# Optimization experiments

Measured on AMD Instinct MI355X. Metric: run time of the kernel, lower is better.

The kernel has to match this reference:

```python
import jax, jax.numpy as jnp
import numpy as np

B, T_AUX, UP = 4, 75, 110
N_AUX, N_Q, HID, SKIP = 54, 256, 192, 256
K, AUX_K = 6, 3
DIL_FACTS = [0, 1, 2] * 3  # dilation_depth=3, dilation_repeat=3
T = T_AUX * UP - 1  # 8249


def conv1d(x, w, b, dil=1, pad=(0, 0)):
    # x: (B,C,T), w: (O,I,K) torch Conv1d layout
    if pad != (0, 0):
        x = jnp.pad(x, ((0, 0), (0, 0), pad))
    y = jax.lax.conv_general_dilated(x, w, (1,), 'VALID', rhs_dilation=(dil,),
                                     dimension_numbers=('NCH', 'OIH', 'NCH'))
    return y + b[None, :, None]


def setup_inputs() -> dict:
    key = jax.random.key(0)
    ks = jax.random.split(key, 24)
    s = 0.05
    inp = {
        'audio': jax.random.normal(ks[0], (B, N_Q, T), jnp.float32),
        'aux': jax.random.normal(ks[1], (B, N_AUX, T_AUX), jnp.float32),
        'scale_in_w': jax.random.normal(ks[2], (N_AUX, N_AUX, 1), jnp.float32) * s,
        'scale_in_b': jax.random.normal(ks[3], (N_AUX,), jnp.float32) * s,
        'aux0_w': jax.random.normal(ks[4], (N_AUX * 3, N_AUX, AUX_K), jnp.float32) * s,
        'aux0_b': jax.random.normal(ks[5], (N_AUX * 3,), jnp.float32) * s,
        'aux1_w': jax.random.normal(ks[6], (N_AUX * 9, N_AUX * 3, AUX_K), jnp.float32) * s,
        'aux1_b': jax.random.normal(ks[7], (N_AUX * 9,), jnp.float32) * s,
        'up_w': jax.random.normal(ks[8], (UP,), jnp.float32) * s,
        'up_b': jax.random.normal(ks[9], (), jnp.float32) * s,
        'causal_w': jax.random.normal(ks[10], (HID, N_Q, K), jnp.float32) * s,
        'causal_b': jax.random.normal(ks[11], (HID,), jnp.float32) * s,
        'inx_w': jax.random.normal(ks[12], (9, 2 * HID, N_AUX * 9, 1), jnp.float32) * s,
        'inx_b': jax.random.normal(ks[13], (9, 2 * HID), jnp.float32) * s,
        'dilh_w': jax.random.normal(ks[14], (9, 2 * HID, HID, K), jnp.float32) * s,
        'dilh_b': jax.random.normal(ks[15], (9, 2 * HID), jnp.float32) * s,
        'skip_w': jax.random.normal(ks[16], (9, SKIP, HID, 1), jnp.float32) * s,
        'skip_b': jax.random.normal(ks[17], (9, SKIP), jnp.float32) * s,
        'out1_w': jax.random.normal(ks[18], (N_Q, SKIP, 1), jnp.float32) * s,
        'out1_b': jax.random.normal(ks[19], (N_Q,), jnp.float32) * s,
        'out2_w': jax.random.normal(ks[20], (N_Q, N_Q, 1), jnp.float32) * s,
        'out2_b': jax.random.normal(ks[21], (N_Q,), jnp.float32) * s,
    }
    return inp


def reference(audio, aux, scale_in_w, scale_in_b, aux0_w, aux0_b, aux1_w, aux1_b,
              up_w, up_b, causal_w, causal_b, inx_w, inx_b, dilh_w, dilh_b,
              skip_w, skip_b, out1_w, out1_b, out2_w, out2_b):
    # conditioning path: scale_in -> two-sided dilated convs -> deconv upsample
    a = conv1d(aux, scale_in_w, scale_in_b)
    a = conv1d(a, aux0_w, aux0_b, dil=1, pad=(1, 1))      # k=3, dil=1, same length
    a = conv1d(a, aux1_w, aux1_b, dil=3, pad=(3, 3))      # k=3, dil=3, same length
    b_, c_, t_ = a.shape
    x = (a[:, :, :, None] * up_w).reshape(b_, c_, t_ * UP) + up_b  # ConvTranspose2d(1,1,(1,UP))
    x = x[:, :, 1:]  # (B, 486, T)
    # audio path: causal conv (left pad k-1) + softsign
    h = jax.nn.soft_sign(conv1d(audio, causal_w, causal_b, dil=1, pad=(K - 1, 0)))
    sum_out = None
    for l, d in enumerate(DIL_FACTS):
        dil = K ** d
        lpad = dil * (K - 1)  # k**(d+1) - k**d
        xh = conv1d(x, inx_w[l], inx_b[l]) * conv1d(h, dilh_w[l], dilh_b[l], dil=dil, pad=(lpad, 0))
        z = jax.nn.sigmoid(xh[:, :HID])
        h = (1.0 - z) * jnp.tanh(xh[:, HID:]) + z * h
        skip = conv1d(h, skip_w[l], skip_b[l])
        sum_out = skip if sum_out is None else sum_out + skip
    out = conv1d(jax.nn.relu(sum_out), out1_w, out1_b)
    out = conv1d(jax.nn.relu(out), out2_w, out2_b)
    return out.transpose(0, 2, 1)  # (B, T, n_quantize)
```

## Files before the change

### kernel.cpp

```cpp
#include <hip/hip_runtime.h>

#define TLEN 8249
#define TPAD 8320
#define NTILES 130
#define NTILES2 65
#define NB 4
#define NAUX 54
#define NQ 256
#define HID 192
#define NSKIP 256
#define KW 6
#define UPF 110
#define TAUX 75
#define PADR 180
#define HROWS (PADR + TPAD)

typedef __attribute__((ext_vector_type(8))) short bf16x8v;
typedef __attribute__((ext_vector_type(4))) float f32x4;

__device__ __forceinline__ unsigned short f2bf(float f) {
  unsigned int u = __float_as_uint(f);
  u += 0x7FFFu + ((u >> 16) & 1u);
  return (unsigned short)(u >> 16);
}

__device__ __forceinline__ f32x4 mfma16(bf16x8v a, bf16x8v b, f32x4 c) {
  return __builtin_amdgcn_mfma_f32_16x16x32_bf16(a, b, c, 0, 0, 0);
}

__global__ void prepack_kernel(
    const float* causal_w, const float* dilh_w, const float* skip_w,
    const float* out1_w, const float* out2_w,
    const float* inx_w, const float* inx_b, const float* up_b,
    unsigned short* pk_causal, unsigned short* pk_dilh, unsigned short* pk_skip,
    unsigned short* pk_out1, unsigned short* pk_out2, float* Cbuf)
{
  int i = blockIdx.x * blockDim.x + threadIdx.x;
  if (i < 9*6*6*24*64*8) {
    int t = i;
    int j = t & 7; t >>= 3;
    int lane = t & 63; t >>= 6;
    int nf = t % 24; t /= 24;
    int kc = t % 6; t /= 6;
    int tap = t % 6; t /= 6;
    int l = t;
    int oc = nf*16 + (lane & 15);
    int ic = kc*32 + ((lane >> 4) << 3) + j;
    pk_dilh[i] = f2bf(dilh_w[((l*384 + oc)*HID + ic)*KW + tap]);
  }
  if (i < 6*8*12*64*8) {
    int t = i;
    int j = t & 7; t >>= 3;
    int lane = t & 63; t >>= 6;
    int nf = t % 12; t /= 12;
    int kc = t % 8; t /= 8;
    int tap = t;
    int oc = nf*16 + (lane & 15);
    int ic = kc*32 + ((lane >> 4) << 3) + j;
    pk_causal[i] = f2bf(causal_w[(oc*NQ + ic)*KW + tap]);
  }
  if (i < 9*6*16*64*8) {
    int t = i;
    int j = t & 7; t >>= 3;
    int lane = t & 63; t >>= 6;
    int nf = t % 16; t /= 16;
    int kc = t % 6; t /= 6;
    int l = t;
    int sc = nf*16 + (lane & 15);
    int ic = kc*32 + ((lane >> 4) << 3) + j;
    pk_skip[i] = f2bf(skip_w[(l*NSKIP + sc)*HID + ic]);
  }
  if (i < 8*16*64*8) {
    int t = i;
    int j = t & 7; t >>= 3;
    int lane = t & 63; t >>= 6;
    int nf = t % 16; t /= 16;
    int kc = t;
    int oq = nf*16 + (lane & 15);
    int sc = kc*32 + ((lane >> 4) << 3) + j;
    pk_out1[i] = f2bf(out1_w[oq*NSKIP + sc]);
    pk_out2[i] = f2bf(out2_w[oq*NQ + sc]);
  }
  if (i < 9*384) {
    int l = i / 384, oc = i % 384;
    const float* wr = inx_w + (l*384 + oc)*486;
    float s = 0.f;
    for (int c = 0; c < 486; c++) s += wr[c];
    Cbuf[i] = up_b[0]*s + inx_b[i];
  }
}

__global__ void zpad_kernel(unsigned short* h_all) {
  int i = blockIdx.x*blockDim.x + threadIdx.x;
  if (i < 9*NB*PADR*HID) {
    int slab = i / (NB*PADR*HID), r = i % (NB*PADR*HID);
    int b = r / (PADR*HID), rr = r % (PADR*HID);
    h_all[((size_t)slab*NB + b)*HROWS*HID + rr] = 0;
  }
}

__global__ void aux1_kernel(const float* aux, const float* w, const float* bias, float* a1) {
  int q = blockIdx.x, b = blockIdx.y, co = threadIdx.x;
  if (co >= NAUX) return;
  float acc = bias[co];
  for (int ci = 0; ci < NAUX; ci++)
    acc += w[co*NAUX + ci] * aux[(b*NAUX + ci)*TAUX + q];
  a1[(b*NAUX + co)*TAUX + q] = acc;
}

__global__ void aux2_kernel(const float* a1, const float* w, const float* bias, float* a2) {
  __shared__ float s[3][NAUX];
  int q = blockIdx.x, b = blockIdx.y, tid = threadIdx.x;
  for (int i = tid; i < 3*NAUX; i += blockDim.x) {
    int k = i / NAUX, c = i % NAUX;
    int qq = q - 1 + k;
    s[k][c] = (qq >= 0 && qq < TAUX) ? a1[(b*NAUX + c)*TAUX + qq] : 0.f;
  }
  __syncthreads();
  int co = tid;
  if (co >= 162) return;
  float acc = bias[co];
  for (int c = 0; c < NAUX; c++)
    #pragma unroll
    for (int k = 0; k < 3; k++)
      acc += w[(co*NAUX + c)*3 + k] * s[k][c];
  a2[(b*162 + co)*TAUX + q] = acc;
}

__global__ void aux3_kernel(const float* a2, const float* w, const float* bias, float* a3) {
  __shared__ float s[3][162];
  int q = blockIdx.x, b = blockIdx.y, tid = threadIdx.x;
  for (int i = tid; i < 3*162; i += blockDim.x) {
    int k = i / 162, c = i % 162;
    int qq = q + 3*(k - 1);
    s[k][c] = (qq >= 0 && qq < TAUX) ? a2[(b*162 + c)*TAUX + qq] : 0.f;
  }
  __syncthreads();
  int co = tid;
  if (co >= 486) return;
  float acc = bias[co];
  for (int c = 0; c < 162; c++)
    #pragma unroll
    for (int k = 0; k < 3; k++)
      acc += w[(co*162 + c)*3 + k] * s[k][c];
  a3[(b*486 + co)*TAUX + q] = acc;
}

__global__ void g_kernel(const float* a3, const float* inx_w, float* G) {
  __shared__ float s[486][15];
  int q0 = blockIdx.x * 15, b = blockIdx.y, l = blockIdx.z;
  int tid = threadIdx.x;
  for (int i = tid; i < 486*15; i += 384) {
    int c = i / 15, qq = i % 15;
    s[c][qq] = a3[(b*486 + c)*TAUX + q0 + qq];
  }
  __syncthreads();
  int oc = tid;
  float acc[15];
  #pragma unroll
  for (int qq = 0; qq < 15; qq++) acc[qq] = 0.f;
  const float* wrow = inx_w + (l*384 + oc)*486;
  for (int c = 0; c < 486; c++) {
    float w = wrow[c];
    #pragma unroll
    for (int qq = 0; qq < 15; qq++) acc[qq] += w * s[c][qq];
  }
  for (int qq = 0; qq < 15; qq++)
    G[((size_t)(l*NB + b)*TAUX + q0 + qq)*384 + oc] = acc[qq];
}

__global__ __launch_bounds__(256, 2)
void causal_kernel(const float* audio, const unsigned short* pk, const float* cb,
                   unsigned short* hbf)
{
  __shared__ __align__(16) unsigned short sA[72*264];
  int b = blockIdx.y, t0 = blockIdx.x*64, tid = threadIdx.x;
  int wv = tid >> 6, lane = tid & 63, lanelo = lane & 15, lanehi = lane >> 4;

  for (int i = tid; i < 72*256; i += 256) {
    int ic = i / 72, tt = i % 72;
    int t = t0 - 5 + tt;
    float v = (t >= 0 && t < TLEN) ? audio[(size_t)(b*NQ + ic)*TLEN + t] : 0.f;
    sA[tt*264 + ic] = f2bf(v);
  }
  __syncthreads();

  f32x4 acc[4][3];
  f32x4 z4 = {0.f, 0.f, 0.f, 0.f};
  #pragma unroll
  for (int m = 0; m < 4; m++)
    #pragma unroll
    for (int i = 0; i < 3; i++) acc[m][i] = z4;

  for (int tap = 0; tap < 6; tap++) {
    for (int kc = 0; kc < 8; kc++) {
      bf16x8v A[4];
      int ko = kc*32 + (lanehi << 3);
      #pragma unroll
      for (int m = 0; m < 4; m++)
        A[m] = *(const bf16x8v*)&sA[(m*16 + lanelo + tap)*264 + ko];
      #pragma unroll
      for (int i = 0; i < 3; i++) {
        int nf = wv*3 + i;
        bf16x8v Bf = *(const bf16x8v*)&pk[(size_t)((((tap*8) + kc)*12 + nf)*64 + lane)*8];
        #pragma unroll
        for (int m = 0; m < 4; m++) acc[m][i] = mfma16(A[m], Bf, acc[m][i]);
      }
    }
  }

  unsigned short hv[4][3][4];
  #pragma unroll
  for (int m = 0; m < 4; m++)
    #pragma unroll
    for (int i = 0; i < 3; i++) {
      int oc = (wv*3 + i)*16 + lanelo;
      float bias = cb[oc];
      #pragma unroll
      for (int r = 0; r < 4; r++) {
        float v = acc[m][i][r] + bias;
        hv[m][i][r] = f2bf(v / (1.f + fabsf(v)));
      }
    }
  __syncthreads();
  #pragma unroll
  for (int m = 0; m < 4; m++)
    #pragma unroll
    for (int i = 0; i < 3; i++) {
      int oc = (wv*3 + i)*16 + lanelo;
      int cbh = oc >> 3, jh = oc & 7;
      #pragma unroll
      for (int r = 0; r < 4; r++) {
        int tl = m*16 + (lanehi << 2) + r;
        sA[tl*192 + ((cbh ^ (tl&7))<<3) + jh] = hv[m][i][r];
      }
    }
  __syncthreads();
  #pragma unroll
  for (int j = 0; j < 6; j++) {
    int c = tid + j*256, row = c/24, cbk = c%24;
    uint4 v = *(const uint4*)&sA[row*192 + ((cbk ^ (row&7))<<3)];
    *(uint4*)&hbf[(size_t)(b*HROWS + t0 + row + PADR)*HID + cbk*8] = v;
  }
}

__global__ __launch_bounds__(512, 2)
void layer_kernel(int dil,
                  const unsigned short* __restrict__ hin,
                  unsigned short* __restrict__ hout,
                  const unsigned short* __restrict__ pk_dilh_l,
                  const float* __restrict__ dilh_b_l,
                  const float* __restrict__ Gl, const float* __restrict__ Cl,
                  const float* __restrict__ up_w)
{
  extern __shared__ __align__(16) unsigned short flat[];
  int b = blockIdx.y, t0 = blockIdx.x*128, tid = threadIdx.x;
  int wv = tid >> 6, lane = tid & 63, lanelo = lane & 15, lanehi = lane >> 4;
  int mwv = wv >> 2, nwv = wv & 3;

  const size_t hbase = (size_t)b * HROWS * HID;
  int rowbase0 = t0 - 5*dil + PADR;
  int W = 128 + 5*dil;

  for (int c = tid; c < W*24; c += 512) {
    int row = c/24, cbk = c%24;
    uint4 v = *(const uint4*)&hin[hbase + (size_t)(rowbase0+row)*HID + cbk*8];
    *(uint4*)&flat[row*192 + ((cbk ^ (row&7))<<3)] = v;
  }
  __syncthreads();

  f32x4 accz[4][3], acct[4][3];
  f32x4 z4 = {0.f, 0.f, 0.f, 0.f};
  #pragma unroll
  for (int m = 0; m < 4; m++)
    #pragma unroll
    for (int i = 0; i < 3; i++) { accz[m][i] = z4; acct[m][i] = z4; }

  for (int tap = 0; tap < 6; tap++) {
    #pragma unroll
    for (int kc = 0; kc < 6; kc++) {
      bf16x8v A[4];
      #pragma unroll
      for (int m = 0; m < 4; m++) {
        int r = mwv*64 + m*16 + lanelo + tap*dil;
        int cbk = kc*4 + lanehi;
        A[m] = *(const bf16x8v*)&flat[r*192 + ((cbk ^ (r&7))<<3)];
      }
      #pragma unroll
      for (int i = 0; i < 3; i++) {
        const unsigned short* bp =
            &pk_dilh_l[(size_t)(((tap*6 + kc)*24 + nwv*3 + i)*64 + lane)*8];
        bf16x8v Bz = *(const bf16x8v*)bp;
        bf16x8v Bt = *(const bf16x8v*)(bp + 12*512);
        #pragma unroll
        for (int m = 0; m < 4; m++) {
          accz[m][i] = mfma16(A[m], Bz, accz[m][i]);
          acct[m][i] = mfma16(A[m], Bt, acct[m][i]);
        }
      }
    }
  }

  float izc[3], itc[3], bzc[3], btc[3];
  #pragma unroll
  for (int i = 0; i < 3; i++) {
    int ocz = (nwv*3 + i)*16 + lanelo;
    izc[i] = Cl[ocz];       itc[i] = Cl[192 + ocz];
    bzc[i] = dilh_b_l[ocz]; btc[i] = dilh_b_l[192 + ocz];
  }
  unsigned short hnv[4][4][3];
  #pragma unroll
  for (int m = 0; m < 4; m++) {
    #pragma unroll
    for (int r = 0; r < 4; r++) {
      int tl = mwv*64 + m*16 + (lanehi << 2) + r;
      int t = t0 + tl;
      int hr = tl + 5*dil;
      int tp1 = t + 1;
      int q = tp1 / UPF; if (q > TAUX - 1) q = TAUX - 1;
      int ui = tp1 - q*UPF; if (ui > UPF - 1) ui = UPF - 1;
      float u = up_w[ui];
      const float* Gb = Gl + (size_t)(b*TAUX + q)*384;
      #pragma unroll
      for (int i = 0; i < 3; i++) {
        int ocz = (nwv*3 + i)*16 + lanelo;
        float iz = u*Gb[ocz]       + izc[i];
        float it = u*Gb[192 + ocz] + itc[i];
        float xz = (accz[m][i][r] + bzc[i]) * iz;
        float xt = (acct[m][i][r] + btc[i]) * it;
        float z  = 1.f / (1.f + __expf(-xz));
        float e2 = __expf(2.f*xt);
        float th = 1.f - 2.f/(e2 + 1.f);
        int cbh = ocz >> 3, jh = ocz & 7;
        unsigned short hob = flat[hr*192 + ((cbh ^ (hr&7))<<3) + jh];
        float hold = __uint_as_float(((unsigned int)hob) << 16);
        hnv[m][r][i] = f2bf((1.f - z)*th + z*hold);
      }
    }
  }
  __syncthreads();
  #pragma unroll
  for (int m = 0; m < 4; m++) {
    #pragma unroll
    for (int r = 0; r < 4; r++) {
      int tl = mwv*64 + m*16 + (lanehi << 2) + r;
      #pragma unroll
      for (int i = 0; i < 3; i++) {
        int ocz = (nwv*3 + i)*16 + lanelo;
        int cbh = ocz >> 3, jh = ocz & 7;
        flat[tl*192 + ((cbh ^ (tl&7))<<3) + jh] = hnv[m][r][i];
      }
    }
  }
  __syncthreads();
  #pragma unroll
  for (int j = 0; j < 6; j++) {
    int c = tid + j*512, row = c/24, cbk = c%24;
    uint4 v = *(const uint4*)&flat[row*192 + ((cbk ^ (row&7))<<3)];
    *(uint4*)&hout[hbase + (size_t)(t0 + row + PADR)*HID + cbk*8] = v;
  }
}

__global__ __launch_bounds__(512, 2)
void tail_kernel(const unsigned short* __restrict__ h_all,
                 const unsigned short* __restrict__ pk_skip,
                 const float* __restrict__ skip_b,
                 const unsigned short* __restrict__ pk1, const float* __restrict__ b1,
                 const unsigned short* __restrict__ pk2, const float* __restrict__ b2,
                 float* __restrict__ dout)
{
  extern __shared__ __align__(16) unsigned short ss[];
  int b = blockIdx.y, t0 = blockIdx.x*128, tid = threadIdx.x;
  int wv = tid >> 6, lane = tid & 63, lanelo = lane & 15, lanehi = lane >> 4;
  int mwv = wv >> 2, nwv = wv & 3;
  const size_t HS = (size_t)NB * HROWS * HID;

  auto hsrc = [&](int l) {
    int slab = (l == 8) ? 0 : (l + 1);
    return h_all + (size_t)slab*HS + (size_t)b*HROWS*HID + (size_t)(t0 + PADR)*HID;
  };

  uint4 st[6];
  {
    const unsigned short* src = hsrc(0);
    #pragma unroll
    for (int j = 0; j < 6; j++) {
      int c = tid + j*512, row = c/24, cbk = c%24;
      st[j] = *(const uint4*)&src[(size_t)row*HID + cbk*8];
    }
    #pragma unroll
    for (int j = 0; j < 6; j++) {
      int c = tid + j*512, row = c/24, cbk = c%24;
      *(uint4*)&ss[row*192 + ((cbk ^ (row&7))<<3)] = st[j];
    }
  }

  f32x4 acc[4][4];
  f32x4 z4 = {0.f, 0.f, 0.f, 0.f};
  #pragma unroll
  for (int m = 0; m < 4; m++)
    #pragma unroll
    for (int i = 0; i < 4; i++) acc[m][i] = z4;

  for (int l = 0; l < 9; l++) {
    __syncthreads();
    if (l < 8) {
      const unsigned short* src = hsrc(l + 1);
      #pragma unroll
      for (int j = 0; j < 6; j++) {
        int c = tid + j*512, row = c/24, cbk = c%24;
        st[j] = *(const uint4*)&src[(size_t)row*HID + cbk*8];
      }
    }
    const unsigned short* bufc = ss + (l & 1)*(128*192);
    #pragma unroll
    for (int kc = 0; kc < 6; kc++) {
      bf16x8v A[4];
      #pragma unroll
      for (int m = 0; m < 4; m++) {
        int r = mwv*64 + m*16 + lanelo;
        int cbk = kc*4 + lanehi;
        A[m] = *(const bf16x8v*)&bufc[r*192 + ((cbk ^ (r&7))<<3)];
      }
      #pragma unroll
      for (int i = 0; i < 4; i++) {
        bf16x8v Bf = *(const bf16x8v*)
            &pk_skip[(size_t)(((l*6 + kc)*16 + nwv*4 + i)*64 + lane)*8];
        #pragma unroll
        for (int m = 0; m < 4; m++) acc[m][i] = mfma16(A[m], Bf, acc[m][i]);
      }
    }
    if (l < 8) {
      unsigned short* bufn = ss + ((l+1) & 1)*(128*192);
      #pragma unroll
      for (int j = 0; j < 6; j++) {
        int c = tid + j*512, row = c/24, cbk = c%24;
        *(uint4*)&bufn[row*192 + ((cbk ^ (row&7))<<3)] = st[j];
      }
    }
  }
  __syncthreads();

  #pragma unroll
  for (int i = 0; i < 4; i++) {
    int sc = (nwv*4 + i)*16 + lanelo;
    float bias = 0.f;
    #pragma unroll
    for (int l = 0; l < 9; l++) bias += skip_b[l*NSKIP + sc];
    #pragma unroll
    for (int m = 0; m < 4; m++) {
      #pragma unroll
      for (int r = 0; r < 4; r++) {
        int tl = mwv*64 + m*16 + (lanehi << 2) + r;
        float v = acc[m][i][r] + bias;
        ss[tl*264 + sc] = f2bf(fmaxf(v, 0.f));
      }
    }
  }
  __syncthreads();

  #pragma unroll
  for (int m = 0; m < 4; m++)
    #pragma unroll
    for (int i = 0; i < 4; i++) acc[m][i] = z4;
  for (int kc = 0; kc < 8; kc++) {
    bf16x8v A[4];
    int ko = kc*32 + (lanehi << 3);
    #pragma unroll
    for (int m = 0; m < 4; m++)
      A[m] = *(const bf16x8v*)&ss[(mwv*64 + m*16 + lanelo)*264 + ko];
    #pragma unroll
    for (int i = 0; i < 4; i++) {
      bf16x8v Bf = *(const bf16x8v*)&pk1[(size_t)((kc*16 + nwv*4 + i)*64 + lane)*8];
      #pragma unroll
      for (int m = 0; m < 4; m++) acc[m][i] = mfma16(A[m], Bf, acc[m][i]);
    }
  }
  __syncthreads();
  #pragma unroll
  for (int m = 0; m < 4; m++)
    #pragma unroll
    for (int i = 0; i < 4; i++) {
      int oq = (nwv*4 + i)*16 + lanelo;
      float bias = b1[oq];
      #pragma unroll
      for (int r = 0; r < 4; r++) {
        int tl = mwv*64 + m*16 + (lanehi << 2) + r;
        float v = acc[m][i][r] + bias;
        ss[tl*264 + oq] = f2bf(fmaxf(v, 0.f));
      }
    }
  __syncthreads();

  #pragma unroll
  for (int m = 0; m < 4; m++)
    #pragma unroll
    for (int i = 0; i < 4; i++) acc[m][i] = z4;
  for (int kc = 0; kc < 8; kc++) {
    bf16x8v A[4];
    int ko = kc*32 + (lanehi << 3);
    #pragma unroll
    for (int m = 0; m < 4; m++)
      A[m] = *(const bf16x8v*)&ss[(mwv*64 + m*16 + lanelo)*264 + ko];
    #pragma unroll
    for (int i = 0; i < 4; i++) {
      bf16x8v Bf = *(const bf16x8v*)&pk2[(size_t)((kc*16 + nwv*4 + i)*64 + lane)*8];
      #pragma unroll
      for (int m = 0; m < 4; m++) acc[m][i] = mfma16(A[m], Bf, acc[m][i]);
    }
  }
  float* so2 = (float*)ss;
  #pragma unroll
  for (int p = 0; p < 2; p++) {
    __syncthreads();
    if (mwv == p) {
      #pragma unroll
      for (int m = 0; m < 4; m++) {
        #pragma unroll
        for (int i = 0; i < 4; i++) {
          int oq = (nwv*4 + i)*16 + lanelo;
          float bias = b2[oq];
          #pragma unroll
          for (int r = 0; r < 4; r++) {
            int lr = m*16 + (lanehi << 2) + r;
            so2[lr*260 + oq] = acc[m][i][r] + bias;
          }
        }
      }
    }
    __syncthreads();
    #pragma unroll
    for (int j = 0; j < 8; j++) {
      int c = tid + j*512, row = c >> 6, ch = c & 63;
      int t = t0 + p*64 + row;
      if (t < TLEN) {
        uint4 v = *(const uint4*)&so2[row*260 + ch*4];
        *(uint4*)&dout[(size_t)(b*TLEN + t)*NQ + ch*4] = v;
      }
    }
  }
}

extern "C" void kernel_launch(void* const* d_in, const int* in_sizes, int n_in,
                              void* d_out, int out_size, void* d_ws, size_t ws_size,
                              hipStream_t stream)
{
  const float* audio      = (const float*)d_in[0];
  const float* aux        = (const float*)d_in[1];
  const float* scale_in_w = (const float*)d_in[2];
  const float* scale_in_b = (const float*)d_in[3];
  const float* aux0_w     = (const float*)d_in[4];
  const float* aux0_b     = (const float*)d_in[5];
  const float* aux1_w     = (const float*)d_in[6];
  const float* aux1_b     = (const float*)d_in[7];
  const float* up_w       = (const float*)d_in[8];
  const float* up_b       = (const float*)d_in[9];
  const float* causal_w   = (const float*)d_in[10];
  const float* causal_b   = (const float*)d_in[11];
  const float* inx_w      = (const float*)d_in[12];
  const float* inx_b      = (const float*)d_in[13];
  const float* dilh_w     = (const float*)d_in[14];
  const float* dilh_b     = (const float*)d_in[15];
  const float* skip_w     = (const float*)d_in[16];
  const float* skip_b     = (const float*)d_in[17];
  const float* out1_w     = (const float*)d_in[18];
  const float* out1_b     = (const float*)d_in[19];
  const float* out2_w     = (const float*)d_in[20];
  const float* out2_b     = (const float*)d_in[21];

  char* ws = (char*)d_ws;
  size_t off = 0;
  auto alloc = [&](size_t bytes) -> void* {
    void* p = ws + off;
    off += (bytes + 255) & ~(size_t)255;
    return p;
  };
  unsigned short* pk_causal = (unsigned short*)alloc((size_t)6*8*12*64*8*2);
  unsigned short* pk_dilh   = (unsigned short*)alloc((size_t)9*6*6*24*64*8*2);
  unsigned short* pk_skip   = (unsigned short*)alloc((size_t)9*6*16*64*8*2);
  unsigned short* pk_out1   = (unsigned short*)alloc((size_t)8*16*64*8*2);
  unsigned short* pk_out2   = (unsigned short*)alloc((size_t)8*16*64*8*2);
  float* Cbuf    = (float*)alloc((size_t)9*384*4);
  float* a1      = (float*)alloc((size_t)NB*NAUX*TAUX*4);
  float* a2      = (float*)alloc((size_t)NB*162*TAUX*4);
  float* a3      = (float*)alloc((size_t)NB*486*TAUX*4);
  float* Gbuf    = (float*)alloc((size_t)9*NB*TAUX*384*4);
  const size_t HS = (size_t)NB*HROWS*HID;
  unsigned short* h_all = (unsigned short*)alloc((size_t)9*HS*2);

  hipFuncSetAttribute((const void*)layer_kernel,
                      hipFuncAttributeMaxDynamicSharedMemorySize, 120000);
  hipFuncSetAttribute((const void*)tail_kernel,
                      hipFuncAttributeMaxDynamicSharedMemorySize, 98304);

  hipLaunchKernelGGL(prepack_kernel, dim3((9*6*6*24*64*8 + 255)/256), dim3(256), 0, stream,
                     causal_w, dilh_w, skip_w, out1_w, out2_w, inx_w, inx_b, up_b,
                     pk_causal, pk_dilh, pk_skip, pk_out1, pk_out2, Cbuf);
  hipLaunchKernelGGL(zpad_kernel, dim3((9*NB*PADR*HID + 255)/256), dim3(256), 0, stream,
                     h_all);
  hipLaunchKernelGGL(aux1_kernel, dim3(TAUX, NB), dim3(64), 0, stream,
                     aux, scale_in_w, scale_in_b, a1);
  hipLaunchKernelGGL(aux2_kernel, dim3(TAUX, NB), dim3(192), 0, stream,
                     a1, aux0_w, aux0_b, a2);
  hipLaunchKernelGGL(aux3_kernel, dim3(TAUX, NB), dim3(512), 0, stream,
                     a2, aux1_w, aux1_b, a3);
  hipLaunchKernelGGL(g_kernel, dim3(5, NB, 9), dim3(384), 0, stream,
                     a3, inx_w, Gbuf);
  hipLaunchKernelGGL(causal_kernel, dim3(NTILES, NB), dim3(256), 0, stream,
                     audio, pk_causal, causal_b, h_all );

  const int dils[9] = {1, 6, 36, 1, 6, 36, 1, 6, 36};
  for (int l = 0; l < 9; l++) {
    const unsigned short* hin = h_all + (size_t)l*HS;
    unsigned short* hout      = (l == 8) ? h_all : h_all + (size_t)(l+1)*HS;
    int ldsb = (128 + 5*dils[l]) * 192 * 2;
    hipLaunchKernelGGL(layer_kernel, dim3(NTILES2, NB), dim3(512), ldsb, stream,
                       dils[l], hin, hout,
                       pk_dilh + (size_t)l*6*6*24*64*8,
                       dilh_b + (size_t)l*384,
                       Gbuf + (size_t)l*NB*TAUX*384,
                       Cbuf + (size_t)l*384,
                       up_w);
  }

  hipLaunchKernelGGL(tail_kernel, dim3(NTILES2, NB), dim3(512), 98304, stream,
                     h_all, pk_skip, skip_b, pk_out1, out1_b, pk_out2, out2_b,
                     (float*)d_out);
}
```

Baseline: 991.7 us.

## Fuse all WaveNet layers and tail into one persistent kernel with grid barriers

Replaces the nine per-layer launches and the separate tail kernel with one persistent kernel of 208 blocks. Each block keeps its 160-step tile of h resident in LDS across layers and accumulates the skip projection in registers. Between layers it writes the tile to a ping-pong global slab and syncs via an atomic grid barrier; only the dilation halo is reloaded. This removes launch overhead and the nine-slab write-then-reread of h for the tail, but depends on all blocks being co-resident and serializes layers on barrier latency, with fewer blocks than the earlier 260-block launches.

Result: slower. 1.191 ms (+20.1%).

```diff
diff --git a/kernel.cpp b/kernel.cpp
--- a/kernel.cpp
+++ b/kernel.cpp
@@ -2,8 +2,9 @@
 
 #define TLEN 8249
 #define TPAD 8320
-#define NTILES 130
-#define NTILES2 65
+#define NTILES_C 130
+#define NTILES_P 52
+#define NBLK (NTILES_P*NB)
 #define NB 4
 #define NAUX 54
 #define NQ 256
@@ -26,6 +27,18 @@
 
 __device__ __forceinline__ f32x4 mfma16(bf16x8v a, bf16x8v b, f32x4 c) {
   return __builtin_amdgcn_mfma_f32_16x16x32_bf16(a, b, c, 0, 0, 0);
+}
+
+__device__ __forceinline__ void gridbar(unsigned int* cnt, unsigned int target, int tid) {
+  __syncthreads();
+  if (tid == 0) {
+    __threadfence();
+    __hip_atomic_fetch_add(cnt, 1u, __ATOMIC_ACQ_REL, __HIP_MEMORY_SCOPE_AGENT);
+    while (__hip_atomic_load(cnt, __ATOMIC_ACQUIRE, __HIP_MEMORY_SCOPE_AGENT) < target)
+      __builtin_amdgcn_s_sleep(2);
+    __threadfence();
+  }
+  __syncthreads();
 }
 
 __global__ void prepack_kernel(
@@ -90,12 +103,12 @@
   }
 }
 
-__global__ void zpad_kernel(unsigned short* h_all) {
+__global__ void zpad_kernel(unsigned short* s0, unsigned short* s1) {
   int i = blockIdx.x*blockDim.x + threadIdx.x;
-  if (i < 9*NB*PADR*HID) {
-    int slab = i / (NB*PADR*HID), r = i % (NB*PADR*HID);
-    int b = r / (PADR*HID), rr = r % (PADR*HID);
-    h_all[((size_t)slab*NB + b)*HROWS*HID + rr] = 0;
+  if (i < NB*PADR*HID) {
+    int b = i / (PADR*HID), rr = i % (PADR*HID);
+    s0[(size_t)b*HROWS*HID + rr] = 0;
+    s1[(size_t)b*HROWS*HID + rr] = 0;
   }
 }
 
@@ -244,200 +257,153 @@
   }
 }
 
-__global__ __launch_bounds__(512, 2)
-void layer_kernel(int dil,
-                  const unsigned short* __restrict__ hin,
-                  unsigned short* __restrict__ hout,
-                  const unsigned short* __restrict__ pk_dilh_l,
-                  const float* __restrict__ dilh_b_l,
-                  const float* __restrict__ Gl, const float* __restrict__ Cl,
-                  const float* __restrict__ up_w)
+__global__ __launch_bounds__(512)
+void wavenet_kernel(const unsigned short* __restrict__ pk_dilh,
+                    const float* __restrict__ dilh_b,
+                    const unsigned short* __restrict__ pk_skip,
+                    const float* __restrict__ skip_b,
+                    const unsigned short* __restrict__ pk1, const float* __restrict__ b1,
+                    const unsigned short* __restrict__ pk2, const float* __restrict__ b2,
+                    const float* __restrict__ Gbuf, const float* __restrict__ Cbuf,
+                    const float* __restrict__ up_w,
+                    unsigned short* __restrict__ slab0,
+                    unsigned short* __restrict__ slab1,
+                    float* __restrict__ dout, unsigned int* cnt)
 {
-  extern __shared__ __align__(16) unsigned short flat[];
-  int b = blockIdx.y, t0 = blockIdx.x*128, tid = threadIdx.x;
+  extern __shared__ __align__(16) unsigned short hwin[];
+  int id = blockIdx.x;
+  int b = id / NTILES_P, tile = id % NTILES_P;
+  int t0 = tile * 160;
+  int tid = threadIdx.x;
   int wv = tid >> 6, lane = tid & 63, lanelo = lane & 15, lanehi = lane >> 4;
   int mwv = wv >> 2, nwv = wv & 3;
-
-  const size_t hbase = (size_t)b * HROWS * HID;
-  int rowbase0 = t0 - 5*dil + PADR;
-  int W = 128 + 5*dil;
-
-  for (int c = tid; c < W*24; c += 512) {
-    int row = c/24, cbk = c%24;
-    uint4 v = *(const uint4*)&hin[hbase + (size_t)(rowbase0+row)*HID + cbk*8];
-    *(uint4*)&flat[row*192 + ((cbk ^ (row&7))<<3)] = v;
-  }
-  __syncthreads();
-
-  f32x4 accz[4][3], acct[4][3];
+  const size_t hb = (size_t)b * HROWS * HID;
   f32x4 z4 = {0.f, 0.f, 0.f, 0.f};
-  #pragma unroll
-  for (int m = 0; m < 4; m++)
-    #pragma unroll
-    for (int i = 0; i < 3; i++) { accz[m][i] = z4; acct[m][i] = z4; }
-
-  for (int tap = 0; tap < 6; tap++) {
+
+  for (int c = tid; c < 160*24; c += 512) {
+    int row = c/24, cbk = c%24, lr = 180 + row;
+    uint4 v = *(const uint4*)&slab0[hb + (size_t)(t0 + PADR + row)*HID + cbk*8];
+    *(uint4*)&hwin[lr*192 + ((cbk ^ (lr&7))<<3)] = v;
+  }
+
+  f32x4 sacc[5][4];
+  #pragma unroll
+  for (int m = 0; m < 5; m++)
+    #pragma unroll
+    for (int i = 0; i < 4; i++) sacc[m][i] = z4;
+
+  for (int l = 0; l < 9; l++) {
+    int lm3 = l - (l/3)*3;
+    int dil = (lm3 == 0) ? 1 : ((lm3 == 1) ? 6 : 36);
+    int H = 5*dil;
+    const unsigned short* pkd = pk_dilh + (size_t)l*6*6*24*64*8;
+    const float* db = dilh_b + l*384;
+    const float* Gl = Gbuf + ((size_t)l*NB + b)*TAUX*384;
+    const float* Cl = Cbuf + l*384;
+    unsigned short* cur = (l & 1) ? slab1 : slab0;
+    unsigned short* nxt = (l & 1) ? slab0 : slab1;
+
+    for (int c = tid; c < H*24; c += 512) {
+      int row = c/24, cbk = c%24, lr = 180 - H + row;
+      uint4 v = *(const uint4*)&cur[hb + (size_t)(t0 + PADR - H + row)*HID + cbk*8];
+      *(uint4*)&hwin[lr*192 + ((cbk ^ (lr&7))<<3)] = v;
+    }
+    __syncthreads();
+
+    f32x4 accz[5][3], acct[5][3];
+    #pragma unroll
+    for (int m = 0; m < 5; m++)
+      #pragma unroll
+      for (int i = 0; i < 3; i++) { accz[m][i] = z4; acct[m][i] = z4; }
+    for (int tap = 0; tap < 6; tap++) {
+      #pragma unroll
+      for (int kc = 0; kc < 6; kc++) {
+        bf16x8v A[5];
+        int cbk = kc*4 + lanehi;
+        #pragma unroll
+        for (int m = 0; m < 5; m++) {
+          int r = 180 - H + mwv*80 + m*16 + lanelo + tap*dil;
+          A[m] = *(const bf16x8v*)&hwin[r*192 + ((cbk ^ (r&7))<<3)];
+        }
+        #pragma unroll
+        for (int i = 0; i < 3; i++) {
+          const unsigned short* bp =
+              &pkd[(size_t)(((tap*6 + kc)*24 + nwv*3 + i)*64 + lane)*8];
+          bf16x8v Bz = *(const bf16x8v*)bp;
+          bf16x8v Bt = *(const bf16x8v*)(bp + 12*512);
+          #pragma unroll
+          for (int m = 0; m < 5; m++) {
+            accz[m][i] = mfma16(A[m], Bz, accz[m][i]);
+            acct[m][i] = mfma16(A[m], Bt, acct[m][i]);
+          }
+        }
+      }
+    }
+    __syncthreads();
+
+    float izc[3], itc[3], bzc[3], btc[3];
+    #pragma unroll
+    for (int i = 0; i < 3; i++) {
+      int ocz = (nwv*3 + i)*16 + lanelo;
+      izc[i] = Cl[ocz];  itc[i] = Cl[192 + ocz];
+      bzc[i] = db[ocz];  btc[i] = db[192 + ocz];
+    }
+    #pragma unroll
+    for (int m = 0; m < 5; m++) {
+      #pragma unroll
+      for (int r = 0; r < 4; r++) {
+        int tl = mwv*80 + m*16 + (lanehi << 2) + r;
+        int t = t0 + tl, lr = 180 + tl;
+        int tp1 = t + 1;
+        int q = tp1 / UPF; if (q > TAUX - 1) q = TAUX - 1;
+        int ui = tp1 - q*UPF; if (ui > UPF - 1) ui = UPF - 1;
+        float u = up_w[ui];
+        const float* Gb = Gl + (size_t)q*384;
+        #pragma unroll
+        for (int i = 0; i < 3; i++) {
+          int ocz = (nwv*3 + i)*16 + lanelo;
+          float iz = u*Gb[ocz]       + izc[i];
+          float it = u*Gb[192 + ocz] + itc[i];
+          float xz = (accz[m][i][r] + bzc[i]) * iz;
+          float xt = (acct[m][i][r] + btc[i]) * it;
+          float z  = 1.f / (1.f + __expf(-xz));
+          float e2 = __expf(2.f*xt);
+          float th = 1.f - 2.f/(e2 + 1.f);
+          int idx = lr*192 + (((ocz >> 3) ^ (lr&7)) << 3) + (ocz & 7);
+          float hold = __uint_as_float(((unsigned int)hwin[idx]) << 16);
+          hwin[idx] = f2bf((1.f - z)*th + z*hold);
+        }
+      }
+    }
+    __syncthreads();
+
+    if (l < 8) {
+      for (int c = tid; c < 160*24; c += 512) {
+        int row = c/24, cbk = c%24, lr = 180 + row;
+        uint4 v = *(const uint4*)&hwin[lr*192 + ((cbk ^ (lr&7))<<3)];
+        *(uint4*)&nxt[hb + (size_t)(t0 + PADR + row)*HID + cbk*8] = v;
+      }
+    }
+
+    const unsigned short* pks = pk_skip + (size_t)l*6*16*64*8;
     #pragma unroll
     for (int kc = 0; kc < 6; kc++) {
-      bf16x8v A[4];
-      #pragma unroll
-      for (int m = 0; m < 4; m++) {
-        int r = mwv*64 + m*16 + lanelo + tap*dil;
-        int cbk = kc*4 + lanehi;
-        A[m] = *(const bf16x8v*)&flat[r*192 + ((cbk ^ (r&7))<<3)];
-      }
-      #pragma unroll
-      for (int i = 0; i < 3; i++) {
-        const unsigned short* bp =
-            &pk_dilh_l[(size_t)(((tap*6 + kc)*24 + nwv*3 + i)*64 + lane)*8];
-        bf16x8v Bz = *(const bf16x8v*)bp;
-        bf16x8v Bt = *(const bf16x8v*)(bp + 12*512);
+      bf16x8v A[5];
+      int cbk = kc*4 + lanehi;
+      #pragma unroll
+      for (int m = 0; m < 5; m++) {
+        int r = 180 + mwv*80 + m*16 + lanelo;
+        A[m] = *(const bf16x8v*)&hwin[r*192 + ((cbk ^ (r&7))<<3)];
+      }
+      #pragma unroll
+      for (int i = 0; i < 4; i++) {
+        bf16x8v Bf = *(const bf16x8v*)&pks[(size_t)((kc*16 + nwv*4 + i)*64 + lane)*8];
         #pragma unroll
-        for (int m = 0; m < 4; m++) {
-          accz[m][i] = mfma16(A[m], Bz, accz[m][i]);
-          acct[m][i] = mfma16(A[m], Bt, acct[m][i]);
-        }
-      }
-    }
-  }
-
-  float izc[3], itc[3], bzc[3], btc[3];
-  #pragma unroll
-  for (int i = 0; i < 3; i++) {
-    int ocz = (nwv*3 + i)*16 + lanelo;
-    izc[i] = Cl[ocz];       itc[i] = Cl[192 + ocz];
-    bzc[i] = dilh_b_l[ocz]; btc[i] = dilh_b_l[192 + ocz];
-  }
-  unsigned short hnv[4][4][3];
-  #pragma unroll
-  for (int m = 0; m < 4; m++) {
-    #pragma unroll
-    for (int r = 0; r < 4; r++) {
-      int tl = mwv*64 + m*16 + (lanehi << 2) + r;
-      int t = t0 + tl;
-      int hr = tl + 5*dil;
-      int tp1 = t + 1;
-      int q = tp1 / UPF; if (q > TAUX - 1) q = TAUX - 1;
-      int ui = tp1 - q*UPF; if (ui > UPF - 1) ui = UPF - 1;
-      float u = up_w[ui];
-      const float* Gb = Gl + (size_t)(b*TAUX + q)*384;
-      #pragma unroll
-      for (int i = 0; i < 3; i++) {
-        int ocz = (nwv*3 + i)*16 + lanelo;
-        float iz = u*Gb[ocz]       + izc[i];
-        float it = u*Gb[192 + ocz] + itc[i];
-        float xz = (accz[m][i][r] + bzc[i]) * iz;
-        float xt = (acct[m][i][r] + btc[i]) * it;
-        float z  = 1.f / (1.f + __expf(-xz));
-        float e2 = __expf(2.f*xt);
-        float th = 1.f - 2.f/(e2 + 1.f);
-        int cbh = ocz >> 3, jh = ocz & 7;
-        unsigned short hob = flat[hr*192 + ((cbh ^ (hr&7))<<3) + jh];
-        float hold = __uint_as_float(((unsigned int)hob) << 16);
-        hnv[m][r][i] = f2bf((1.f - z)*th + z*hold);
-      }
-    }
-  }
-  __syncthreads();
-  #pragma unroll
-  for (int m = 0; m < 4; m++) {
-    #pragma unroll
-    for (int r = 0; r < 4; r++) {
-      int tl = mwv*64 + m*16 + (lanehi << 2) + r;
-      #pragma unroll
-      for (int i = 0; i < 3; i++) {
-        int ocz = (nwv*3 + i)*16 + lanelo;
-        int cbh = ocz >> 3, jh = ocz & 7;
-        flat[tl*192 + ((cbh ^ (tl&7))<<3) + jh] = hnv[m][r][i];
-      }
-    }
-  }
-  __syncthreads();
-  #pragma unroll
-  for (int j = 0; j < 6; j++) {
-    int c = tid + j*512, row = c/24, cbk = c%24;
-    uint4 v = *(const uint4*)&flat[row*192 + ((cbk ^ (row&7))<<3)];
-    *(uint4*)&hout[hbase + (size_t)(t0 + row + PADR)*HID + cbk*8] = v;
-  }
-}
-
-__global__ __launch_bounds__(512, 2)
-void tail_kernel(const unsigned short* __restrict__ h_all,
-                 const unsigned short* __restrict__ pk_skip,
-                 const float* __restrict__ skip_b,
-                 const unsigned short* __restrict__ pk1, const float* __restrict__ b1,
-                 const unsigned short* __restrict__ pk2, const float* __restrict__ b2,
-                 float* __restrict__ dout)
-{
-  extern __shared__ __align__(16) unsigned short ss[];
-  int b = blockIdx.y, t0 = blockIdx.x*128, tid = threadIdx.x;
-  int wv = tid >> 6, lane = tid & 63, lanelo = lane & 15, lanehi = lane >> 4;
-  int mwv = wv >> 2, nwv = wv & 3;
-  const size_t HS = (size_t)NB * HROWS * HID;
-
-  auto hsrc = [&](int l) {
-    int slab = (l == 8) ? 0 : (l + 1);
-    return h_all + (size_t)slab*HS + (size_t)b*HROWS*HID + (size_t)(t0 + PADR)*HID;
-  };
-
-  uint4 st[6];
-  {
-    const unsigned short* src = hsrc(0);
-    #pragma unroll
-    for (int j = 0; j < 6; j++) {
-      int c = tid + j*512, row = c/24, cbk = c%24;
-      st[j] = *(const uint4*)&src[(size_t)row*HID + cbk*8];
-    }
-    #pragma unroll
-    for (int j = 0; j < 6; j++) {
-      int c = tid + j*512, row = c/24, cbk = c%24;
-      *(uint4*)&ss[row*192 + ((cbk ^ (row&7))<<3)] = st[j];
-    }
-  }
-
-  f32x4 acc[4][4];
-  f32x4 z4 = {0.f, 0.f, 0.f, 0.f};
-  #pragma unroll
-  for (int m = 0; m < 4; m++)
-    #pragma unroll
-    for (int i = 0; i < 4; i++) acc[m][i] = z4;
-
-  for (int l = 0; l < 9; l++) {
-    __syncthreads();
-    if (l < 8) {
-      const unsigned short* src = hsrc(l + 1);
-      #pragma unroll
-      for (int j = 0; j < 6; j++) {
-        int c = tid + j*512, row = c/24, cbk = c%24;
-        st[j] = *(const uint4*)&src[(size_t)row*HID + cbk*8];
-      }
-    }
-    const unsigned short* bufc = ss + (l & 1)*(128*192);
-    #pragma unroll
-    for (int kc = 0; kc < 6; kc++) {
-      bf16x8v A[4];
-      #pragma unroll
-      for (int m = 0; m < 4; m++) {
-        int r = mwv*64 + m*16 + lanelo;
-        int cbk = kc*4 + lanehi;
-        A[m] = *(const bf16x8v*)&bufc[r*192 + ((cbk ^ (r&7))<<3)];
-      }
-      #pragma unroll
-      for (int i = 0; i < 4; i++) {
-        bf16x8v Bf = *(const bf16x8v*)
-            &pk_skip[(size_t)(((l*6 + kc)*16 + nwv*4 + i)*64 + lane)*8];
-        #pragma unroll
-        for (int m = 0; m < 4; m++) acc[m][i] = mfma16(A[m], Bf, acc[m][i]);
-      }
-    }
-    if (l < 8) {
-      unsigned short* bufn = ss + ((l+1) & 1)*(128*192);
-      #pragma unroll
-      for (int j = 0; j < 6; j++) {
-        int c = tid + j*512, row = c/24, cbk = c%24;
-        *(uint4*)&bufn[row*192 + ((cbk ^ (row&7))<<3)] = st[j];
-      }
-    }
+        for (int m = 0; m < 5; m++) sacc[m][i] = mfma16(A[m], Bf, sacc[m][i]);
+      }
+    }
+
+    if (l < 8) gridbar(cnt, (unsigned)NBLK*(l+1), tid);
   }
   __syncthreads();
 
@@ -448,91 +414,89 @@
     #pragma unroll
     for (int l = 0; l < 9; l++) bias += skip_b[l*NSKIP + sc];
     #pragma unroll
-    for (int m = 0; m < 4; m++) {
+    for (int m = 0; m < 5; m++) {
       #pragma unroll
       for (int r = 0; r < 4; r++) {
-        int tl = mwv*64 + m*16 + (lanehi << 2) + r;
-        float v = acc[m][i][r] + bias;
-        ss[tl*264 + sc] = f2bf(fmaxf(v, 0.f));
-      }
-    }
-  }
-  __syncthreads();
-
-  #pragma unroll
-  for (int m = 0; m < 4; m++)
-    #pragma unroll
-    for (int i = 0; i < 4; i++) acc[m][i] = z4;
+        int tl = mwv*80 + m*16 + (lanehi << 2) + r;
+        float v = sacc[m][i][r] + bias;
+        hwin[tl*264 + sc] = f2bf(fmaxf(v, 0.f));
+      }
+    }
+  }
+  __syncthreads();
+
+  f32x4 oacc[5][4];
+  #pragma unroll
+  for (int m = 0; m < 5; m++)
+    #pragma unroll
+    for (int i = 0; i < 4; i++) oacc[m][i] = z4;
   for (int kc = 0; kc < 8; kc++) {
-    bf16x8v A[4];
+    bf16x8v A[5];
     int ko = kc*32 + (lanehi << 3);
     #pragma unroll
-    for (int m = 0; m < 4; m++)
-      A[m] = *(const bf16x8v*)&ss[(mwv*64 + m*16 + lanelo)*264 + ko];
+    for (int m = 0; m < 5; m++)
+      A[m] = *(const bf16x8v*)&hwin[(mwv*80 + m*16 + lanelo)*264 + ko];
     #pragma unroll
     for (int i = 0; i < 4; i++) {
       bf16x8v Bf = *(const bf16x8v*)&pk1[(size_t)((kc*16 + nwv*4 + i)*64 + lane)*8];
       #pragma unroll
-      for (int m = 0; m < 4; m++) acc[m][i] = mfma16(A[m], Bf, acc[m][i]);
-    }
-  }
-  __syncthreads();
-  #pragma unroll
-  for (int m = 0; m < 4; m++)
+      for (int m = 0; m < 5; m++) oacc[m][i] = mfma16(A[m], Bf, oacc[m][i]);
+    }
+  }
+  __syncthreads();
+  #pragma unroll
+  for (int m = 0; m < 5; m++)
     #pragma unroll
     for (int i = 0; i < 4; i++) {
       int oq = (nwv*4 + i)*16 + lanelo;
       float bias = b1[oq];
       #pragma unroll
       for (int r = 0; r < 4; r++) {
-        int tl = mwv*64 + m*16 + (lanehi << 2) + r;
-        float v = acc[m][i][r] + bias;
-        ss[tl*264 + oq] = f2bf(fmaxf(v, 0.f));
-      }
-    }
-  __syncthreads();
-
-  #pragma unroll
-  for (int m = 0; m < 4; m++)
-    #pragma unroll
-    for (int i = 0; i < 4; i++) acc[m][i] = z4;
+        int tl = mwv*80 + m*16 + (lanehi << 2) + r;
+        hwin[tl*264 + oq] = f2bf(fmaxf(oacc[m][i][r] + bias, 0.f));
+      }
+    }
+  __syncthreads();
+
+  #pragma unroll
+  for (int m = 0; m < 5; m++)
+    #pragma unroll
+    for (int i = 0; i < 4; i++) oacc[m][i] = z4;
   for (int kc = 0; kc < 8; kc++) {
-    bf16x8v A[4];
+    bf16x8v A[5];
     int ko = kc*32 + (lanehi << 3);
     #pragma unroll
-    for (int m = 0; m < 4; m++)
-      A[m] = *(const bf16x8v*)&ss[(mwv*64 + m*16 + lanelo)*264 + ko];
+    for (int m = 0; m < 5; m++)
+      A[m] = *(const bf16x8v*)&hwin[(mwv*80 + m*16 + lanelo)*264 + ko];
     #pragma unroll
     for (int i = 0; i < 4; i++) {
       bf16x8v Bf = *(const bf16x8v*)&pk2[(size_t)((kc*16 + nwv*4 + i)*64 + lane)*8];
       #pragma unroll
-      for (int m = 0; m < 4; m++) acc[m][i] = mfma16(A[m], Bf, acc[m][i]);
-    }
-  }
-  float* so2 = (float*)ss;
+      for (int m = 0; m < 5; m++) oacc[m][i] = mfma16(A[m], Bf, oacc[m][i]);
+    }
+  }
+  float* so2 = (float*)hwin;
   #pragma unroll
   for (int p = 0; p < 2; p++) {
     __syncthreads();
     if (mwv == p) {
       #pragma unroll
-      for (int m = 0; m < 4; m++) {
+      for (int m = 0; m < 5; m++)
         #pragma unroll
         for (int i = 0; i < 4; i++) {
           int oq = (nwv*4 + i)*16 + lanelo;
           float bias = b2[oq];
           #pragma unroll
           for (int r = 0; r < 4; r++) {
-            int lr = m*16 + (lanehi << 2) + r;
-            so2[lr*260 + oq] = acc[m][i][r] + bias;
+            int lrr = m*16 + (lanehi << 2) + r;
+            so2[lrr*260 + oq] = oacc[m][i][r] + bias;
           }
         }
-      }
     }
     __syncthreads();
-    #pragma unroll
-    for (int j = 0; j < 8; j++) {
-      int c = tid + j*512, row = c >> 6, ch = c & 63;
-      int t = t0 + p*64 + row;
+    for (int c = tid; c < 80*64; c += 512) {
+      int row = c >> 6, ch = c & 63;
+      int t = t0 + p*80 + row;
       if (t < TLEN) {
         uint4 v = *(const uint4*)&so2[row*260 + ch*4];
         *(uint4*)&dout[(size_t)(b*TLEN + t)*NQ + ch*4] = v;
@@ -586,18 +550,19 @@
   float* a3      = (float*)alloc((size_t)NB*486*TAUX*4);
   float* Gbuf    = (float*)alloc((size_t)9*NB*TAUX*384*4);
   const size_t HS = (size_t)NB*HROWS*HID;
-  unsigned short* h_all = (unsigned short*)alloc((size_t)9*HS*2);
-
-  hipFuncSetAttribute((const void*)layer_kernel,
-                      hipFuncAttributeMaxDynamicSharedMemorySize, 120000);
-  hipFuncSetAttribute((const void*)tail_kernel,
-                      hipFuncAttributeMaxDynamicSharedMemorySize, 98304);
-
+  unsigned short* slab0 = (unsigned short*)alloc(HS*2);
+  unsigned short* slab1 = (unsigned short*)alloc(HS*2);
+  unsigned int* cnt = (unsigned int*)alloc(256);
+
+  hipFuncSetAttribute((const void*)wavenet_kernel,
+                      hipFuncAttributeMaxDynamicSharedMemorySize, 340*192*2);
+
+  hipMemsetAsync(cnt, 0, 4, stream);
   hipLaunchKernelGGL(prepack_kernel, dim3((9*6*6*24*64*8 + 255)/256), dim3(256), 0, stream,
                      causal_w, dilh_w, skip_w, out1_w, out2_w, inx_w, inx_b, up_b,
                      pk_causal, pk_dilh, pk_skip, pk_out1, pk_out2, Cbuf);
-  hipLaunchKernelGGL(zpad_kernel, dim3((9*NB*PADR*HID + 255)/256), dim3(256), 0, stream,
-                     h_all);
+  hipLaunchKernelGGL(zpad_kernel, dim3((NB*PADR*HID + 255)/256), dim3(256), 0, stream,
+                     slab0, slab1);
   hipLaunchKernelGGL(aux1_kernel, dim3(TAUX, NB), dim3(64), 0, stream,
                      aux, scale_in_w, scale_in_b, a1);
   hipLaunchKernelGGL(aux2_kernel, dim3(TAUX, NB), dim3(192), 0, stream,
@@ -606,24 +571,11 @@
                      a2, aux1_w, aux1_b, a3);
   hipLaunchKernelGGL(g_kernel, dim3(5, NB, 9), dim3(384), 0, stream,
                      a3, inx_w, Gbuf);
-  hipLaunchKernelGGL(causal_kernel, dim3(NTILES, NB), dim3(256), 0, stream,
-                     audio, pk_causal, causal_b, h_all );
-
-  const int dils[9] = {1, 6, 36, 1, 6, 36, 1, 6, 36};
-  for (int l = 0; l < 9; l++) {
-    const unsigned short* hin = h_all + (size_t)l*HS;
-    unsigned short* hout      = (l == 8) ? h_all : h_all + (size_t)(l+1)*HS;
-    int ldsb = (128 + 5*dils[l]) * 192 * 2;
-    hipLaunchKernelGGL(layer_kernel, dim3(NTILES2, NB), dim3(512), ldsb, stream,
-                       dils[l], hin, hout,
-                       pk_dilh + (size_t)l*6*6*24*64*8,
-                       dilh_b + (size_t)l*384,
-                       Gbuf + (size_t)l*NB*TAUX*384,
-                       Cbuf + (size_t)l*384,
-                       up_w);
-  }
-
-  hipLaunchKernelGGL(tail_kernel, dim3(NTILES2, NB), dim3(512), 98304, stream,
-                     h_all, pk_skip, skip_b, pk_out1, out1_b, pk_out2, out2_b,
-                     (float*)d_out);
-}
+  hipLaunchKernelGGL(causal_kernel, dim3(NTILES_C, NB), dim3(256), 0, stream,
+                     audio, pk_causal, causal_b, slab0);
+
+  hipLaunchKernelGGL(wavenet_kernel, dim3(NBLK), dim3(512), 340*192*2, stream,
+                     pk_dilh, dilh_b, pk_skip, skip_b,
+                     pk_out1, out1_b, pk_out2, out2_b,
+                     Gbuf, Cbuf, up_w, slab0, slab1, (float*)d_out, cnt);
+}
```
